# Kernel tuning notes

Hardware: AMD Instinct MI355X
Metric: run time of the kernel (lower is better)

Reference implementation:

```python
import jax, jax.numpy as jnp
import numpy as np

S, E, H, D, F = 2048, 1280, 16, 80, 5120
EPS = 1e-6


def _ln(x, g, b):
    m = x.mean(-1, keepdims=True)
    v = x.var(-1, keepdims=True)
    return (x - m) * jax.lax.rsqrt(v + EPS) * g + b


def _rotate_half(x):
    x1, x2 = jnp.split(x, 2, axis=-1)
    return jnp.concatenate([-x2, x1], axis=-1)


def _quick_gelu(x):
    return x * jax.nn.sigmoid(1.702 * x)


def setup_inputs() -> dict:
    key = jax.random.key(0)
    ks = jax.random.split(key, 12)
    inp = {
        "hidden_states": jax.random.normal(ks[0], (S, E), jnp.float32),
        "attention_mask": jnp.ones((1, 1, S, S), jnp.bool_),
        "cos": jax.random.uniform(ks[1], (S, D), jnp.float32),
        "sin": jax.random.uniform(ks[2], (S, D), jnp.float32),
        "ln1_g": jnp.ones((E,), jnp.float32),
        "ln1_b": jnp.zeros((E,), jnp.float32),
        "ln2_g": jnp.ones((E,), jnp.float32),
        "ln2_b": jnp.zeros((E,), jnp.float32),
        "w_qkv": jax.random.normal(ks[3], (E, 3 * E), jnp.float32) * (E ** -0.5),
        "b_qkv": jax.random.normal(ks[4], (3 * E,), jnp.float32) * 0.02,
        "w_o": jax.random.normal(ks[5], (E, E), jnp.float32) * (E ** -0.5),
        "b_o": jax.random.normal(ks[6], (E,), jnp.float32) * 0.02,
        "w_fc1": jax.random.normal(ks[7], (E, F), jnp.float32) * (E ** -0.5),
        "b_fc1": jax.random.normal(ks[8], (F,), jnp.float32) * 0.02,
        "w_fc2": jax.random.normal(ks[9], (F, E), jnp.float32) * (F ** -0.5),
        "b_fc2": jax.random.normal(ks[10], (E,), jnp.float32) * 0.02,
    }
    return inp


def reference(hidden_states, attention_mask, cos, sin, ln1_g, ln1_b, ln2_g, ln2_b,
              w_qkv, b_qkv, w_o, b_o, w_fc1, b_fc1, w_fc2, b_fc2):
    x = hidden_states  # [S, E]
    h = _ln(x, ln1_g, ln1_b)
    qkv = h @ w_qkv + b_qkv  # [S, 3E]
    q, k, v = jnp.split(qkv, 3, axis=-1)
    q = q.reshape(S, H, D)
    k = k.reshape(S, H, D)
    v = v.reshape(S, H, D)
    # rotary in fp32, cos/sin broadcast over head axis: [S, 1, D]
    c = cos[:, None, :].astype(jnp.float32)
    s = sin[:, None, :].astype(jnp.float32)
    qf, kf = q.astype(jnp.float32), k.astype(jnp.float32)
    q = (qf * c + _rotate_half(qf) * s).astype(q.dtype)
    k = (kf * c + _rotate_half(kf) * s).astype(k.dtype)
    # attention scores [H, S, S]
    scores = jnp.einsum('shd,thd->hst', q, k) / np.float32(np.sqrt(D))
    scores = jnp.where(attention_mask[0], scores, jnp.finfo(scores.dtype).min)
    probs = jax.nn.softmax(scores.astype(jnp.float32), axis=-1).astype(q.dtype)
    attn = jnp.einsum('hst,thd->shd', probs, v).reshape(S, E)
    attn = attn @ w_o + b_o
    x = x + attn
    h2 = _ln(x, ln2_g, ln2_b)
    mlp = _quick_gelu(h2 @ w_fc1 + b_fc1) @ w_fc2 + b_fc2
    return x + mlp
```

## Files before the change

kernel.cpp:

```cpp
#include <hip/hip_runtime.h>
#include <stdint.h>
#include <math.h>

#define S_LEN 2048
#define EMB   1280
#define NHEAD 16
#define HDIM  80
#define FDIM  5120

typedef __bf16 bf16x8 __attribute__((ext_vector_type(8)));
typedef float  f32x4  __attribute__((ext_vector_type(4)));
typedef int    i32x4  __attribute__((ext_vector_type(4)));
typedef unsigned short u16x8 __attribute__((ext_vector_type(8)));
typedef unsigned short u16x4 __attribute__((ext_vector_type(4)));

__device__ __forceinline__ float b2f(unsigned short u) {
    union { float f; unsigned int i; } x; x.i = ((unsigned int)u) << 16; return x.f;
}
__device__ __forceinline__ unsigned short f2b(float f) {
    union { float f; unsigned int i; } x; x.f = f;
    unsigned int r = x.i + 0x7FFFu + ((x.i >> 16) & 1u);
    return (unsigned short)(r >> 16);
}

__device__ __forceinline__ float wave_rsum(float v) {
    #pragma unroll
    for (int o = 32; o; o >>= 1) v += __shfl_down(v, o);
    return v;
}

__device__ __forceinline__ void trans64(
    const float* __restrict__ in, unsigned short* __restrict__ out,
    int R, int C, int bx, int by, int tid)
{
    __shared__ unsigned short tile[64][65];
    int c0 = bx * 64, r0 = by * 64;
    int tx = tid & 63, ty = tid >> 6;
    #pragma unroll
    for (int j = 0; j < 16; ++j) {
        int row = ty + j * 4;
        tile[row][tx] = f2b(in[(size_t)(r0 + row) * C + c0 + tx]);
    }
    __syncthreads();
    #pragma unroll
    for (int j = 0; j < 16; ++j) {
        int row = ty + j * 4;
        out[(size_t)(c0 + row) * R + r0 + tx] = tile[tx][row];
    }
}

__global__ __launch_bounds__(256) void transpose4_kernel(
    const float* __restrict__ w_qkv, unsigned short* __restrict__ wT_qkv,
    const float* __restrict__ w_o,   unsigned short* __restrict__ wT_o,
    const float* __restrict__ w_fc1, unsigned short* __restrict__ wT_fc1,
    const float* __restrict__ w_fc2, unsigned short* __restrict__ wT_fc2)
{
    int id = blockIdx.x, tid = threadIdx.x;
    if (id < 1200) {
        trans64(w_qkv, wT_qkv, 1280, 3840, id % 60, id / 60, tid);
    } else if (id < 1600) {
        int t = id - 1200;
        trans64(w_o, wT_o, 1280, 1280, t % 20, t / 20, tid);
    } else if (id < 3200) {
        int t = id - 1600;
        trans64(w_fc1, wT_fc1, 1280, 5120, t % 80, t / 80, tid);
    } else {
        int t = id - 3200;
        trans64(w_fc2, wT_fc2, 5120, 1280, t % 20, t / 20, tid);
    }
}

__global__ __launch_bounds__(256) void ln_kernel(
    const float* __restrict__ x,
    const float* __restrict__ g,
    const float* __restrict__ b,
    unsigned short* __restrict__ out)
{
    int row = blockIdx.x, tid = threadIdx.x;
    int lane = tid & 63, wave = tid >> 6;
    const float* xr = x + (size_t)row * EMB;
    float v[5], s = 0.f, ss = 0.f;
    #pragma unroll
    for (int i = 0; i < 5; ++i) {
        float f = xr[tid + i * 256];
        v[i] = f; s += f; ss += f * f;
    }
    s = wave_rsum(s); ss = wave_rsum(ss);
    __shared__ float rs[4], rss[4];
    if (lane == 0) { rs[wave] = s; rss[wave] = ss; }
    __syncthreads();
    float st  = rs[0] + rs[1] + rs[2] + rs[3];
    float sst = rss[0] + rss[1] + rss[2] + rss[3];
    float mean = st * (1.0f / EMB);
    float var  = sst * (1.0f / EMB) - mean * mean;
    float inv  = rsqrtf(var + 1e-6f);
    unsigned short* orow = out + (size_t)row * EMB;
    #pragma unroll
    for (int i = 0; i < 5; ++i) {
        int c = tid + i * 256;
        orow[c] = f2b((v[i] - mean) * inv * g[c] + b[c]);
    }
}

template<int EPI, int OM, int SPLIT>
__global__ __launch_bounds__(256) void gemm_kernel(
    const unsigned short* __restrict__ A,
    const unsigned short* __restrict__ Bt,
    const float* __restrict__ bias,
    const float* __restrict__ res,
    void* __restrict__ Cv,
    int M, int N, int K)
{
    __shared__ __align__(16) unsigned short As[2][128 * 32];
    __shared__ __align__(16) unsigned short Bs[2][128 * 32];

    int tid = threadIdx.x;
    int lane = tid & 63, wave = tid >> 6;
    int m0 = blockIdx.x * 128, n0 = blockIdx.y * 128;
    int wm = (wave >> 1) * 64, wn = (wave & 1) * 64;
    int kc = K / SPLIT;
    int kbeg = blockIdx.z * kc;
    const int NITER = kc / 32;

    f32x4 acc[4][4];
    #pragma unroll
    for (int i = 0; i < 4; ++i)
        #pragma unroll
        for (int j = 0; j < 4; ++j)
            acc[i][j] = (f32x4){0.f, 0.f, 0.f, 0.f};

    const unsigned short* Ap0 = A  + (size_t)(m0 + (tid >> 2)) * K + (tid & 3) * 8 + kbeg;
    const unsigned short* Ap1 = Ap0 + (size_t)64 * K;
    const unsigned short* Bp0 = Bt + (size_t)(n0 + (tid >> 2)) * K + (tid & 3) * 8 + kbeg;
    const unsigned short* Bp1 = Bp0 + (size_t)64 * K;

    int arow = lane & 15, aq = (lane >> 4) * 8;
    int aoff[4], boff[4];
    #pragma unroll
    for (int i = 0; i < 4; ++i) {
        aoff[i] = (wm + i * 16 + arow) * 32 + aq;
        boff[i] = (wn + i * 16 + arow) * 32 + aq;
    }

    i32x4 rA0a, rA1a, rB0a, rB1a, rA0b, rA1b, rB0b, rB1b;

    rA0b = *(const i32x4*)(Ap0);
    rA1b = *(const i32x4*)(Ap1);
    rB0b = *(const i32x4*)(Bp0);
    rB1b = *(const i32x4*)(Bp1);
    *(i32x4*)&As[0][tid * 8]        = rA0b;
    *(i32x4*)&As[0][2048 + tid * 8] = rA1b;
    *(i32x4*)&Bs[0][tid * 8]        = rB0b;
    *(i32x4*)&Bs[0][2048 + tid * 8] = rB1b;
    if (NITER > 1) {
        rA0a = *(const i32x4*)(Ap0 + 32);
        rA1a = *(const i32x4*)(Ap1 + 32);
        rB0a = *(const i32x4*)(Bp0 + 32);
        rB1a = *(const i32x4*)(Bp1 + 32);
    }
    __syncthreads();

#define GSTEP(IT, AW0, AW1, BW0, BW1, AL0, AL1, BL0, BL1)                    \
    {                                                                         \
        const int cur = (IT) & 1, nb = cur ^ 1;                               \
        if ((IT) + 1 < NITER) {                                               \
            *(i32x4*)&As[nb][tid * 8]        = AW0;                           \
            *(i32x4*)&As[nb][2048 + tid * 8] = AW1;                           \
            *(i32x4*)&Bs[nb][tid * 8]        = BW0;                           \
            *(i32x4*)&Bs[nb][2048 + tid * 8] = BW1;                           \
        }                                                                     \
        if ((IT) + 2 < NITER) {                                               \
            int ko = ((IT) + 2) * 32;                                         \
            AL0 = *(const i32x4*)(Ap0 + ko);                                  \
            AL1 = *(const i32x4*)(Ap1 + ko);                                  \
            BL0 = *(const i32x4*)(Bp0 + ko);                                  \
            BL1 = *(const i32x4*)(Bp1 + ko);                                  \
        }                                                                     \
        bf16x8 af[4], bfm[4];                                                 \
        _Pragma("unroll") for (int i = 0; i < 4; ++i) {                       \
            af[i]  = *(const bf16x8*)&As[cur][aoff[i]];                       \
            bfm[i] = *(const bf16x8*)&Bs[cur][boff[i]];                       \
        }                                                                     \
        _Pragma("unroll") for (int mi = 0; mi < 4; ++mi)                      \
            _Pragma("unroll") for (int ni = 0; ni < 4; ++ni)                  \
                acc[mi][ni] = __builtin_amdgcn_mfma_f32_16x16x32_bf16(        \
                    af[mi], bfm[ni], acc[mi][ni], 0, 0, 0);                   \
        __syncthreads();                                                      \
    }

    for (int it = 0; it < NITER; it += 2) {
        GSTEP(it,     rA0a, rA1a, rB0a, rB1a, rA0b, rA1b, rB0b, rB1b)
        GSTEP(it + 1, rA0b, rA1b, rB0b, rB1b, rA0a, rA1a, rB0a, rB1a)
    }
#undef GSTEP

    int col = lane & 15;
    int rbase = (lane >> 4) * 4;
    #pragma unroll
    for (int ni = 0; ni < 4; ++ni) {
        int gn = n0 + wn + ni * 16 + col;
        float bv = (OM == 2) ? 0.f : bias[gn];
        #pragma unroll
        for (int mi = 0; mi < 4; ++mi) {
            int gm = m0 + wm + mi * 16 + rbase;
            #pragma unroll
            for (int r = 0; r < 4; ++r) {
                float v = acc[mi][ni][r] + bv;
                if (OM != 2) {
                    if (EPI == 1) v = v / (1.0f + expf(-1.702f * v));
                }
                if (OM == 2)
                    ((float*)Cv)[((size_t)blockIdx.z * M + gm + r) * N + gn] = v;
                else if (OM == 1)
                    ((float*)Cv)[(size_t)(gm + r) * N + gn] = v;
                else
                    ((unsigned short*)Cv)[(size_t)(gm + r) * N + gn] = f2b(v);
            }
        }
    }
}

template<int Z>
__global__ __launch_bounds__(256) void reduceZ_kernel(
    const float* __restrict__ part,
    const float* __restrict__ res,
    const float* __restrict__ bias,
    float* __restrict__ out)
{
    size_t i4 = ((size_t)blockIdx.x * 256 + threadIdx.x) * 4;
    int colb = (int)(i4 % EMB);
    f32x4 a = *(const f32x4*)&res[i4];
    f32x4 bv = *(const f32x4*)&bias[colb];
    a += bv;
    const size_t slice = (size_t)S_LEN * EMB;
    #pragma unroll
    for (int z = 0; z < Z; ++z)
        a += *(const f32x4*)&part[z * slice + i4];
    *(f32x4*)&out[i4] = a;
}

__global__ __launch_bounds__(256) void ropev_kernel(
    const unsigned short* __restrict__ qkv,
    const float* __restrict__ cosb,
    const float* __restrict__ sinb,
    unsigned short* __restrict__ q_out,
    unsigned short* __restrict__ k_out,
    unsigned short* __restrict__ vt)
{
    __shared__ unsigned short qT[64 * 84];
    __shared__ unsigned short kT[64 * 84];
    __shared__ unsigned short vT[64 * 84];

    int h = blockIdx.x >> 5, stile = blockIdx.x & 31;
    int s0 = stile * 64;
    int tid = threadIdx.x;

    u16x4 qr[5], kr[5];
    #pragma unroll
    for (int i = 0; i < 5; ++i) {
        int u = tid + i * 256;
        int row = u / 20, col = (u % 20) * 4;
        const unsigned short* base = qkv + (size_t)(s0 + row) * (3 * EMB) + h * HDIM + col;
        qr[i] = *(const u16x4*)base;
        kr[i] = *(const u16x4*)(base + EMB);
        u16x4 v4 = *(const u16x4*)(base + 2 * EMB);
        *(u16x4*)&qT[row * 84 + col] = qr[i];
        *(u16x4*)&kT[row * 84 + col] = kr[i];
        *(u16x4*)&vT[row * 84 + col] = v4;
    }
    __syncthreads();

    #pragma unroll
    for (int i = 0; i < 5; ++i) {
        int u = tid + i * 256;
        int row = u / 20, col = (u % 20) * 4;
        int pcol = (col < 40) ? col + 40 : col - 40;
        float sgn = (col < 40) ? -1.f : 1.f;
        u16x4 qp = *(const u16x4*)&qT[row * 84 + pcol];
        u16x4 kp = *(const u16x4*)&kT[row * 84 + pcol];
        f32x4 c4 = *(const f32x4*)&cosb[(size_t)(s0 + row) * HDIM + col];
        f32x4 s4 = *(const f32x4*)&sinb[(size_t)(s0 + row) * HDIM + col];
        u16x4 qo, ko;
        #pragma unroll
        for (int j = 0; j < 4; ++j) {
            qo[j] = f2b(b2f(qr[i][j]) * c4[j] + sgn * b2f(qp[j]) * s4[j]);
            ko[j] = f2b(b2f(kr[i][j]) * c4[j] + sgn * b2f(kp[j]) * s4[j]);
        }
        size_t o = ((size_t)h * S_LEN + s0 + row) * HDIM + col;
        *(u16x4*)&q_out[o] = qo;
        *(u16x4*)&k_out[o] = ko;
    }
    #pragma unroll
    for (int i = 0; i < 5; ++i) {
        int w = tid + i * 256;
        int d = w >> 4, c4i = (w & 15) * 4;
        u16x4 pk;
        #pragma unroll
        for (int j = 0; j < 4; ++j) pk[j] = vT[(c4i + j) * 84 + d];
        *(u16x4*)(vt + ((size_t)h * HDIM + d) * S_LEN + s0 + c4i) = pk;
    }
}

__global__ __launch_bounds__(256) void fattn_kernel(
    const unsigned short* __restrict__ q,
    const unsigned short* __restrict__ k,
    const unsigned short* __restrict__ vt,
    unsigned short* __restrict__ out)
{
    __shared__ __align__(16) unsigned short Qs[64 * 96];
    __shared__ __align__(16) unsigned short Ks[2][64 * 96];
    __shared__ __align__(16) unsigned short Vs[2][80 * 72];
    __shared__ __align__(16) unsigned short Pt[4 * 16 * 72];

    int tid = threadIdx.x;
    int lane = tid & 63, wave = tid >> 6;
    int arow = lane & 15, quad = lane >> 4;
    int h = blockIdx.x >> 5, qb = blockIdx.x & 31;
    int s0 = qb * 64;
    const float c = 0.16129856f;

    const unsigned short* qbase = q + ((size_t)h * S_LEN + s0) * HDIM;
    const unsigned short* kbase = k + (size_t)h * S_LEN * HDIM;
    const unsigned short* vbase = vt + (size_t)h * HDIM * S_LEN;

    #pragma unroll
    for (int i = 0; i < 5; ++i) {
        int u = tid + i * 256;
        int row = u / 20, col = (u % 20) * 4;
        u16x4 qv = *(const u16x4*)(qbase + u * 4);
        u16x4 qs4;
        #pragma unroll
        for (int j = 0; j < 4; ++j) qs4[j] = f2b(b2f(qv[j]) * c);
        *(u16x4*)&Qs[row * 96 + col] = qs4;
    }
    {
        int zr = tid >> 2, zc = 80 + (tid & 3) * 4;
        *(u16x4*)&Qs[zr * 96 + zc]    = (u16x4){0, 0, 0, 0};
        *(u16x4*)&Ks[0][zr * 96 + zc] = (u16x4){0, 0, 0, 0};
        *(u16x4*)&Ks[1][zr * 96 + zc] = (u16x4){0, 0, 0, 0};
    }

    u16x4 kreg[5], vreg[5];
    #pragma unroll
    for (int i = 0; i < 5; ++i) {
        int u = tid + i * 256;
        kreg[i] = *(const u16x4*)(kbase + u * 4);
        vreg[i] = *(const u16x4*)(vbase + (size_t)(u >> 4) * S_LEN + (u & 15) * 4);
    }
    #pragma unroll
    for (int i = 0; i < 5; ++i) {
        int u = tid + i * 256;
        *(u16x4*)&Ks[0][(u / 20) * 96 + (u % 20) * 4] = kreg[i];
        *(u16x4*)&Vs[0][(u >> 4) * 72 + (u & 15) * 4] = vreg[i];
    }
    #pragma unroll
    for (int i = 0; i < 5; ++i) {
        int u = tid + i * 256;
        kreg[i] = *(const u16x4*)(kbase + (size_t)64 * HDIM + u * 4);
        vreg[i] = *(const u16x4*)(vbase + (size_t)(u >> 4) * S_LEN + 64 + (u & 15) * 4);
    }
    __syncthreads();

    int pw = wave * 16 * 72;
    float l_part = 0.f;
    f32x4 o[5];
    #pragma unroll
    for (int di = 0; di < 5; ++di) o[di] = (f32x4){0.f, 0.f, 0.f, 0.f};

    const int NIT = S_LEN / 64;
    for (int it = 0; it < NIT; ++it) {
        int cur = it & 1;
        if (it + 1 < NIT) {
            int nb = (it + 1) & 1;
            #pragma unroll
            for (int i = 0; i < 5; ++i) {
                int u = tid + i * 256;
                *(u16x4*)&Ks[nb][(u / 20) * 96 + (u % 20) * 4] = kreg[i];
                *(u16x4*)&Vs[nb][(u >> 4) * 72 + (u & 15) * 4] = vreg[i];
            }
        }
        if (it + 2 < NIT) {
            int t0 = (it + 2) * 64;
            #pragma unroll
            for (int i = 0; i < 5; ++i) {
                int u = tid + i * 256;
                kreg[i] = *(const u16x4*)(kbase + (size_t)t0 * HDIM + u * 4);
                vreg[i] = *(const u16x4*)(vbase + (size_t)(u >> 4) * S_LEN + t0 + (u & 15) * 4);
            }
        }

        f32x4 sc[4];
        #pragma unroll
        for (int ni = 0; ni < 4; ++ni) sc[ni] = (f32x4){0.f, 0.f, 0.f, 0.f};
        #pragma unroll
        for (int kk = 0; kk < 3; ++kk) {
            bf16x8 bq = *(const bf16x8*)&Qs[(wave * 16 + arow) * 96 + kk * 32 + quad * 8];
            #pragma unroll
            for (int ni = 0; ni < 4; ++ni) {
                bf16x8 ak = *(const bf16x8*)&Ks[cur][(ni * 16 + arow) * 96 + kk * 32 + quad * 8];
                sc[ni] = __builtin_amdgcn_mfma_f32_16x16x32_bf16(ak, bq, sc[ni], 0, 0, 0);
            }
        }

        #pragma unroll
        for (int ni = 0; ni < 4; ++ni) {
            u16x4 pk;
            #pragma unroll
            for (int r = 0; r < 4; ++r) {
                float p = exp2f(sc[ni][r]);
                l_part += p;
                __bf16 pb = (__bf16)p;
                pk[r] = *(unsigned short*)&pb;
            }
            *(u16x4*)&Pt[pw + arow * 72 + ni * 16 + quad * 4] = pk;
        }

        #pragma unroll
        for (int kk = 0; kk < 2; ++kk) {
            bf16x8 ap = *(const bf16x8*)&Pt[pw + arow * 72 + kk * 32 + quad * 8];
            #pragma unroll
            for (int di = 0; di < 5; ++di) {
                bf16x8 bv = *(const bf16x8*)&Vs[cur][(di * 16 + arow) * 72 + kk * 32 + quad * 8];
                o[di] = __builtin_amdgcn_mfma_f32_16x16x32_bf16(ap, bv, o[di], 0, 0, 0);
            }
        }

        __syncthreads();
    }

    float l_run = l_part;
    l_run += __shfl_xor(l_run, 16);
    l_run += __shfl_xor(l_run, 32);

    float inv[4];
    #pragma unroll
    for (int r = 0; r < 4; ++r)
        inv[r] = 1.f / __shfl(l_run, (lane & 48) | (quad * 4 + r));
    #pragma unroll
    for (int r = 0; r < 4; ++r) {
        int gq = s0 + wave * 16 + quad * 4 + r;
        unsigned short* op = out + (size_t)gq * EMB + h * HDIM;
        #pragma unroll
        for (int di = 0; di < 5; ++di)
            op[di * 16 + arow] = f2b(o[di][r] * inv[r]);
    }
}

extern "C" void kernel_launch(void* const* d_in, const int* in_sizes, int n_in,
                              void* d_out, int out_size, void* d_ws, size_t ws_size,
                              hipStream_t stream)
{
    const float* hidden = (const float*)d_in[0];
    const float* cosb  = (const float*)d_in[2];
    const float* sinb  = (const float*)d_in[3];
    const float* ln1g  = (const float*)d_in[4];
    const float* ln1b  = (const float*)d_in[5];
    const float* ln2g  = (const float*)d_in[6];
    const float* ln2b  = (const float*)d_in[7];
    const float* w_qkv = (const float*)d_in[8];
    const float* b_qkv = (const float*)d_in[9];
    const float* w_o   = (const float*)d_in[10];
    const float* b_o   = (const float*)d_in[11];
    const float* w_fc1 = (const float*)d_in[12];
    const float* b_fc1 = (const float*)d_in[13];
    const float* w_fc2 = (const float*)d_in[14];
    const float* b_fc2 = (const float*)d_in[15];

    char* ws = (char*)d_ws;
    size_t off = 0;
    auto alloc = [&](size_t bytes) -> void* {
        void* p = (void*)(ws + off);
        off += (bytes + 255) & ~(size_t)255;
        return p;
    };
    unsigned short* wT_qkv = (unsigned short*)alloc((size_t)3840 * 1280 * 2);
    unsigned short* wT_o   = (unsigned short*)alloc((size_t)1280 * 1280 * 2);
    unsigned short* wT_fc1 = (unsigned short*)alloc((size_t)5120 * 1280 * 2);
    unsigned short* wT_fc2 = (unsigned short*)alloc((size_t)1280 * 5120 * 2);
    unsigned short* h1     = (unsigned short*)alloc((size_t)S_LEN * EMB * 2);
    unsigned short* qkv    = (unsigned short*)alloc((size_t)S_LEN * 3 * EMB * 2);
    unsigned short* q_r    = (unsigned short*)alloc((size_t)S_LEN * EMB * 2);
    unsigned short* k_r    = (unsigned short*)alloc((size_t)S_LEN * EMB * 2);
    unsigned short* vt_g   = (unsigned short*)alloc((size_t)S_LEN * EMB * 2);
    unsigned short* attn_o = (unsigned short*)alloc((size_t)S_LEN * EMB * 2);
    float*          x1     = (float*)alloc((size_t)S_LEN * EMB * 4);
    unsigned short* h2     = (unsigned short*)alloc((size_t)S_LEN * EMB * 2);
    unsigned short* mlp1   = (unsigned short*)alloc((size_t)S_LEN * FDIM * 2);
    float* partials = (float*)h1;

    transpose4_kernel<<<4800, 256, 0, stream>>>(
        w_qkv, wT_qkv, w_o, wT_o, w_fc1, wT_fc1, w_fc2, wT_fc2);

    ln_kernel<<<S_LEN, 256, 0, stream>>>(hidden, ln1g, ln1b, h1);

    gemm_kernel<0, 0, 1><<<dim3(S_LEN / 128, 3840 / 128, 1), 256, 0, stream>>>(
        h1, wT_qkv, b_qkv, nullptr, qkv, S_LEN, 3 * EMB, EMB);

    ropev_kernel<<<NHEAD * (S_LEN / 64), 256, 0, stream>>>(qkv, cosb, sinb, q_r, k_r, vt_g);

    fattn_kernel<<<NHEAD * (S_LEN / 64), 256, 0, stream>>>(q_r, k_r, vt_g, attn_o);

    gemm_kernel<0, 2, 2><<<dim3(S_LEN / 128, 1280 / 128, 2), 256, 0, stream>>>(
        attn_o, wT_o, b_o, nullptr, partials, S_LEN, EMB, EMB);
    reduceZ_kernel<2><<<(S_LEN * EMB / 4) / 256, 256, 0, stream>>>(
        partials, hidden, b_o, x1);

    ln_kernel<<<S_LEN, 256, 0, stream>>>(x1, ln2g, ln2b, h2);

    gemm_kernel<1, 0, 1><<<dim3(S_LEN / 128, FDIM / 128, 1), 256, 0, stream>>>(
        h2, wT_fc1, b_fc1, nullptr, mlp1, S_LEN, FDIM, EMB);

    gemm_kernel<0, 2, 4><<<dim3(S_LEN / 128, 1280 / 128, 4), 256, 0, stream>>>(
        mlp1, wT_fc2, b_fc2, nullptr, partials, S_LEN, EMB, FDIM);
    reduceZ_kernel<4><<<(S_LEN * EMB / 4) / 256, 256, 0, stream>>>(
        partials, x1, b_fc2, (float*)d_out);
}
```

Measured before the change: 370.9 us.

## Give each attention wave two query tiles and fuse split-K reduce with LayerNorm

The flash attention kernel drops to 128 threads (2 waves), and each wave now handles 32 query rows instead of 16. Each K and V fragment read from LDS therefore feeds two MFMAs, doubling reuse and halving LDS traffic per FLOP, at the cost of more registers, fewer waves per block and occupancy capped by launch bounds (128,1). Separately, the reduction of the output-projection split-K partials, the residual add and LayerNorm2 are fused into one row kernel. This removes one launch and one read of x1.

```diff
diff --git a/kernel.cpp b/kernel.cpp
--- a/kernel.cpp
+++ b/kernel.cpp
@@ -95,6 +95,44 @@
     float var  = sst * (1.0f / EMB) - mean * mean;
     float inv  = rsqrtf(var + 1e-6f);
     unsigned short* orow = out + (size_t)row * EMB;
+    #pragma unroll
+    for (int i = 0; i < 5; ++i) {
+        int c = tid + i * 256;
+        orow[c] = f2b((v[i] - mean) * inv * g[c] + b[c]);
+    }
+}
+
+__global__ __launch_bounds__(256) void reduce2_ln_kernel(
+    const float* __restrict__ part,
+    const float* __restrict__ hidden,
+    const float* __restrict__ bias,
+    const float* __restrict__ g,
+    const float* __restrict__ b,
+    float* __restrict__ x1,
+    unsigned short* __restrict__ h2)
+{
+    int row = blockIdx.x, tid = threadIdx.x;
+    int lane = tid & 63, wave = tid >> 6;
+    const size_t slice = (size_t)S_LEN * EMB;
+    float v[5], s = 0.f, ss = 0.f;
+    #pragma unroll
+    for (int i = 0; i < 5; ++i) {
+        int c = tid + i * 256;
+        size_t idx = (size_t)row * EMB + c;
+        float f = part[idx] + part[slice + idx] + hidden[idx] + bias[c];
+        x1[idx] = f;
+        v[i] = f; s += f; ss += f * f;
+    }
+    s = wave_rsum(s); ss = wave_rsum(ss);
+    __shared__ float rs[4], rss[4];
+    if (lane == 0) { rs[wave] = s; rss[wave] = ss; }
+    __syncthreads();
+    float st  = rs[0] + rs[1] + rs[2] + rs[3];
+    float sst = rss[0] + rss[1] + rss[2] + rss[3];
+    float mean = st * (1.0f / EMB);
+    float var  = sst * (1.0f / EMB) - mean * mean;
+    float inv  = rsqrtf(var + 1e-6f);
+    unsigned short* orow = h2 + (size_t)row * EMB;
     #pragma unroll
     for (int i = 0; i < 5; ++i) {
         int c = tid + i * 256;
@@ -301,7 +339,7 @@
     }
 }
 
-__global__ __launch_bounds__(256) void fattn_kernel(
+__global__ __launch_bounds__(128, 1) void fattn_kernel(
     const unsigned short* __restrict__ q,
     const unsigned short* __restrict__ k,
     const unsigned short* __restrict__ vt,
@@ -310,7 +348,7 @@
     __shared__ __align__(16) unsigned short Qs[64 * 96];
     __shared__ __align__(16) unsigned short Ks[2][64 * 96];
     __shared__ __align__(16) unsigned short Vs[2][80 * 72];
-    __shared__ __align__(16) unsigned short Pt[4 * 16 * 72];
+    __shared__ __align__(16) unsigned short Pt[2 * 32 * 72];
 
     int tid = threadIdx.x;
     int lane = tid & 63, wave = tid >> 6;
@@ -324,8 +362,8 @@
     const unsigned short* vbase = vt + (size_t)h * HDIM * S_LEN;
 
     #pragma unroll
-    for (int i = 0; i < 5; ++i) {
-        int u = tid + i * 256;
+    for (int i = 0; i < 10; ++i) {
+        int u = tid + i * 128;
         int row = u / 20, col = (u % 20) * 4;
         u16x4 qv = *(const u16x4*)(qbase + u * 4);
         u16x4 qs4;
@@ -333,39 +371,44 @@
         for (int j = 0; j < 4; ++j) qs4[j] = f2b(b2f(qv[j]) * c);
         *(u16x4*)&Qs[row * 96 + col] = qs4;
     }
-    {
-        int zr = tid >> 2, zc = 80 + (tid & 3) * 4;
+    #pragma unroll
+    for (int j = 0; j < 2; ++j) {
+        int sx = tid + j * 128;
+        int zr = sx >> 2, zc = 80 + (sx & 3) * 4;
         *(u16x4*)&Qs[zr * 96 + zc]    = (u16x4){0, 0, 0, 0};
         *(u16x4*)&Ks[0][zr * 96 + zc] = (u16x4){0, 0, 0, 0};
         *(u16x4*)&Ks[1][zr * 96 + zc] = (u16x4){0, 0, 0, 0};
     }
 
-    u16x4 kreg[5], vreg[5];
-    #pragma unroll
-    for (int i = 0; i < 5; ++i) {
-        int u = tid + i * 256;
+    u16x4 kreg[10], vreg[10];
+    #pragma unroll
+    for (int i = 0; i < 10; ++i) {
+        int u = tid + i * 128;
         kreg[i] = *(const u16x4*)(kbase + u * 4);
         vreg[i] = *(const u16x4*)(vbase + (size_t)(u >> 4) * S_LEN + (u & 15) * 4);
     }
     #pragma unroll
-    for (int i = 0; i < 5; ++i) {
-        int u = tid + i * 256;
+    for (int i = 0; i < 10; ++i) {
+        int u = tid + i * 128;
         *(u16x4*)&Ks[0][(u / 20) * 96 + (u % 20) * 4] = kreg[i];
         *(u16x4*)&Vs[0][(u >> 4) * 72 + (u & 15) * 4] = vreg[i];
     }
     #pragma unroll
-    for (int i = 0; i < 5; ++i) {
-        int u = tid + i * 256;
+    for (int i = 0; i < 10; ++i) {
+        int u = tid + i * 128;
         kreg[i] = *(const u16x4*)(kbase + (size_t)64 * HDIM + u * 4);
         vreg[i] = *(const u16x4*)(vbase + (size_t)(u >> 4) * S_LEN + 64 + (u & 15) * 4);
     }
     __syncthreads();
 
-    int pw = wave * 16 * 72;
-    float l_part = 0.f;
-    f32x4 o[5];
-    #pragma unroll
-    for (int di = 0; di < 5; ++di) o[di] = (f32x4){0.f, 0.f, 0.f, 0.f};
+    int pw = wave * 32 * 72;
+    float l0 = 0.f, l1 = 0.f;
+    f32x4 o0[5], o1[5];
+    #pragma unroll
+    for (int di = 0; di < 5; ++di) {
+        o0[di] = (f32x4){0.f, 0.f, 0.f, 0.f};
+        o1[di] = (f32x4){0.f, 0.f, 0.f, 0.f};
+    }
 
     const int NIT = S_LEN / 64;
     for (int it = 0; it < NIT; ++it) {
@@ -373,8 +416,8 @@
         if (it + 1 < NIT) {
             int nb = (it + 1) & 1;
             #pragma unroll
-            for (int i = 0; i < 5; ++i) {
-                int u = tid + i * 256;
+            for (int i = 0; i < 10; ++i) {
+                int u = tid + i * 128;
                 *(u16x4*)&Ks[nb][(u / 20) * 96 + (u % 20) * 4] = kreg[i];
                 *(u16x4*)&Vs[nb][(u >> 4) * 72 + (u & 15) * 4] = vreg[i];
             }
@@ -382,67 +425,79 @@
         if (it + 2 < NIT) {
             int t0 = (it + 2) * 64;
             #pragma unroll
-            for (int i = 0; i < 5; ++i) {
-                int u = tid + i * 256;
+            for (int i = 0; i < 10; ++i) {
+                int u = tid + i * 128;
                 kreg[i] = *(const u16x4*)(kbase + (size_t)t0 * HDIM + u * 4);
                 vreg[i] = *(const u16x4*)(vbase + (size_t)(u >> 4) * S_LEN + t0 + (u & 15) * 4);
             }
         }
 
-        f32x4 sc[4];
-        #pragma unroll
-        for (int ni = 0; ni < 4; ++ni) sc[ni] = (f32x4){0.f, 0.f, 0.f, 0.f};
+        f32x4 sa[4], sb[4];
+        #pragma unroll
+        for (int ni = 0; ni < 4; ++ni) {
+            sa[ni] = (f32x4){0.f, 0.f, 0.f, 0.f};
+            sb[ni] = (f32x4){0.f, 0.f, 0.f, 0.f};
+        }
         #pragma unroll
         for (int kk = 0; kk < 3; ++kk) {
-            bf16x8 bq = *(const bf16x8*)&Qs[(wave * 16 + arow) * 96 + kk * 32 + quad * 8];
+            bf16x8 bq0 = *(const bf16x8*)&Qs[(wave * 32 + arow) * 96 + kk * 32 + quad * 8];
+            bf16x8 bq1 = *(const bf16x8*)&Qs[(wave * 32 + 16 + arow) * 96 + kk * 32 + quad * 8];
             #pragma unroll
             for (int ni = 0; ni < 4; ++ni) {
                 bf16x8 ak = *(const bf16x8*)&Ks[cur][(ni * 16 + arow) * 96 + kk * 32 + quad * 8];
-                sc[ni] = __builtin_amdgcn_mfma_f32_16x16x32_bf16(ak, bq, sc[ni], 0, 0, 0);
+                sa[ni] = __builtin_amdgcn_mfma_f32_16x16x32_bf16(ak, bq0, sa[ni], 0, 0, 0);
+                sb[ni] = __builtin_amdgcn_mfma_f32_16x16x32_bf16(ak, bq1, sb[ni], 0, 0, 0);
             }
         }
 
         #pragma unroll
         for (int ni = 0; ni < 4; ++ni) {
-            u16x4 pk;
+            u16x4 pka, pkb;
             #pragma unroll
             for (int r = 0; r < 4; ++r) {
-                float p = exp2f(sc[ni][r]);
-                l_part += p;
-                __bf16 pb = (__bf16)p;
-                pk[r] = *(unsigned short*)&pb;
+                float pa = exp2f(sa[ni][r]);
+                float pb = exp2f(sb[ni][r]);
+                l0 += pa; l1 += pb;
+                __bf16 ba = (__bf16)pa, bb = (__bf16)pb;
+                pka[r] = *(unsigned short*)&ba;
+                pkb[r] = *(unsigned short*)&bb;
             }
-            *(u16x4*)&Pt[pw + arow * 72 + ni * 16 + quad * 4] = pk;
+            *(u16x4*)&Pt[pw + arow * 72 + ni * 16 + quad * 4] = pka;
+            *(u16x4*)&Pt[pw + (16 + arow) * 72 + ni * 16 + quad * 4] = pkb;
         }
 
         #pragma unroll
         for (int kk = 0; kk < 2; ++kk) {
-            bf16x8 ap = *(const bf16x8*)&Pt[pw + arow * 72 + kk * 32 + quad * 8];
+            bf16x8 ap0 = *(const bf16x8*)&Pt[pw + arow * 72 + kk * 32 + quad * 8];
+            bf16x8 ap1 = *(const bf16x8*)&Pt[pw + (16 + arow) * 72 + kk * 32 + quad * 8];
             #pragma unroll
             for (int di = 0; di < 5; ++di) {
                 bf16x8 bv = *(const bf16x8*)&Vs[cur][(di * 16 + arow) * 72 + kk * 32 + quad * 8];
-                o[di] = __builtin_amdgcn_mfma_f32_16x16x32_bf16(ap, bv, o[di], 0, 0, 0);
+                o0[di] = __builtin_amdgcn_mfma_f32_16x16x32_bf16(ap0, bv, o0[di], 0, 0, 0);
+                o1[di] = __builtin_amdgcn_mfma_f32_16x16x32_bf16(ap1, bv, o1[di], 0, 0, 0);
             }
         }
 
         __syncthreads();
     }
 
-    float l_run = l_part;
-    l_run += __shfl_xor(l_run, 16);
-    l_run += __shfl_xor(l_run, 32);
-
-    float inv[4];
-    #pragma unroll
-    for (int r = 0; r < 4; ++r)
-        inv[r] = 1.f / __shfl(l_run, (lane & 48) | (quad * 4 + r));
+    l0 += __shfl_xor(l0, 16); l0 += __shfl_xor(l0, 32);
+    l1 += __shfl_xor(l1, 16); l1 += __shfl_xor(l1, 32);
+
     #pragma unroll
     for (int r = 0; r < 4; ++r) {
-        int gq = s0 + wave * 16 + quad * 4 + r;
-        unsigned short* op = out + (size_t)gq * EMB + h * HDIM;
-        #pragma unroll
-        for (int di = 0; di < 5; ++di)
-            op[di * 16 + arow] = f2b(o[di][r] * inv[r]);
+        int src = (lane & 48) | (quad * 4 + r);
+        float inv0 = 1.f / __shfl(l0, src);
+        float inv1 = 1.f / __shfl(l1, src);
+        int gq0 = s0 + wave * 32 + quad * 4 + r;
+        int gq1 = gq0 + 16;
+        unsigned short* op0 = out + (size_t)gq0 * EMB + h * HDIM;
+        unsigned short* op1 = out + (size_t)gq1 * EMB + h * HDIM;
+        #pragma unroll
+        for (int di = 0; di < 5; ++di) {
+            op0[di * 16 + arow] = f2b(o0[di][r] * inv0);
+            op1[di * 16 + arow] = f2b(o1[di][r] * inv1);
+        }
     }
 }
 
@@ -498,14 +553,12 @@
 
     ropev_kernel<<<NHEAD * (S_LEN / 64), 256, 0, stream>>>(qkv, cosb, sinb, q_r, k_r, vt_g);
 
-    fattn_kernel<<<NHEAD * (S_LEN / 64), 256, 0, stream>>>(q_r, k_r, vt_g, attn_o);
+    fattn_kernel<<<NHEAD * (S_LEN / 64), 128, 0, stream>>>(q_r, k_r, vt_g, attn_o);
 
     gemm_kernel<0, 2, 2><<<dim3(S_LEN / 128, 1280 / 128, 2), 256, 0, stream>>>(
         attn_o, wT_o, b_o, nullptr, partials, S_LEN, EMB, EMB);
-    reduceZ_kernel<2><<<(S_LEN * EMB / 4) / 256, 256, 0, stream>>>(
-        partials, hidden, b_o, x1);
-
-    ln_kernel<<<S_LEN, 256, 0, stream>>>(x1, ln2g, ln2b, h2);
+    reduce2_ln_kernel<<<S_LEN, 256, 0, stream>>>(
+        partials, hidden, b_o, ln2g, ln2b, x1, h2);
 
     gemm_kernel<1, 0, 1><<<dim3(S_LEN / 128, FDIM / 128, 1), 256, 0, stream>>>(
         h2, wT_fc1, b_fc1, nullptr, mlp1, S_LEN, FDIM, EMB);
```

Result: slower. 382.8 us (+3.2%).
